# Optimization experiments

Measured on AMD Instinct MI355X. Metric: run time of the kernel, lower is better.

The kernel has to match this reference:

```python
import jax, jax.numpy as jnp
import numpy as np

D_MODEL = 768
D_POS = 64
NHEAD = 12
D_FF = 3072
HEAD_DIM = D_MODEL // NHEAD
LN_EPS = 1e-5


def _layer_norm(x, gamma, beta):
    mu = jnp.mean(x, axis=-1, keepdims=True)
    var = jnp.var(x, axis=-1, keepdims=True)
    return (x - mu) * jax.lax.rsqrt(var + LN_EPS) * gamma + beta


def setup_inputs() -> dict:
    key = jax.random.key(0)
    ks = jax.random.split(key, 16)
    L, N = 256, 4
    s = 0.02
    return {
        "src": jax.random.normal(ks[0], (L, N, D_MODEL), jnp.float32),
        "pos": jax.random.normal(ks[1], (N, L, L, D_POS), jnp.float32),
        "q_w": jax.random.normal(ks[2], (D_MODEL, D_MODEL), jnp.float32) * s,
        "q_b": jnp.zeros((D_MODEL,), jnp.float32),
        "k_w": jax.random.normal(ks[3], (D_MODEL, D_MODEL), jnp.float32) * s,
        "k_b": jnp.zeros((D_MODEL,), jnp.float32),
        "v_w": jax.random.normal(ks[4], (D_MODEL, D_MODEL), jnp.float32) * s,
        "v_b": jnp.zeros((D_MODEL,), jnp.float32),
        "p_w": jax.random.normal(ks[5], (D_MODEL, D_POS), jnp.float32) * s,
        "p_b": jnp.zeros((D_MODEL,), jnp.float32),
        "out_w": jax.random.normal(ks[6], (D_MODEL, D_MODEL), jnp.float32) * s,
        "out_b": jnp.zeros((D_MODEL,), jnp.float32),
        "lin1_w": jax.random.normal(ks[7], (D_FF, D_MODEL), jnp.float32) * s,
        "lin1_b": jnp.zeros((D_FF,), jnp.float32),
        "lin2_w": jax.random.normal(ks[8], (D_MODEL, D_FF), jnp.float32) * s,
        "lin2_b": jnp.zeros((D_MODEL,), jnp.float32),
        "n1_g": jnp.ones((D_MODEL,), jnp.float32),
        "n1_b": jnp.zeros((D_MODEL,), jnp.float32),
        "n2_g": jnp.ones((D_MODEL,), jnp.float32),
        "n2_b": jnp.zeros((D_MODEL,), jnp.float32),
    }


def reference(src, pos, q_w, q_b, k_w, k_b, v_w, v_b, p_w, p_b,
              out_w, out_b, lin1_w, lin1_b, lin2_w, lin2_b,
              n1_g, n1_b, n2_g, n2_b):
    L, N, E = src.shape
    H, hd = NHEAD, HEAD_DIM
    scaling = float(hd) ** -0.5

    # projections (F.linear: x @ W.T + b)
    q = (src @ q_w.T + q_b).reshape(L, N, H, hd).transpose(1, 2, 0, 3) * scaling  # (N,H,L,hd)
    k = (src @ k_w.T + k_b).reshape(L, N, H, hd).transpose(1, 2, 0, 3)            # (N,H,L,hd)
    v = (src @ v_w.T + v_b).reshape(L, N, H, hd).transpose(1, 2, 0, 3)            # (N,H,L,hd)
    p = (pos @ p_w.T + p_b).reshape(N, L, L, H, hd)                               # (N,L,L,H,hd)

    # content-content + content-position scores
    scores = jnp.einsum('nhid,nhjd->nhij', q, k) \
           + jnp.einsum('nhid,nijhd->nhij', q, p)                                 # (N,H,L,L)
    attn = jax.nn.softmax(scores, axis=-1)

    ctx = jnp.einsum('nhij,nhjd->nhid', attn, v)          # (N,H,L,hd)
    ctx = ctx.transpose(2, 0, 1, 3).reshape(L, N, E)      # (L,N,E)
    attn_out = ctx @ out_w.T + out_b

    x = _layer_norm(src + attn_out, n1_g, n1_b)
    ff = jax.nn.gelu(x @ lin1_w.T + lin1_b, approximate=False) @ lin2_w.T + lin2_b
    x = _layer_norm(x + ff, n2_g, n2_b)
    return x
```

## Files before the change

### kernel.cpp

```cpp
#include <hip/hip_runtime.h>
#include <hip/hip_bf16.h>
#include <math.h>

typedef __hip_bfloat16 bf16;
typedef unsigned short u16;
typedef __attribute__((ext_vector_type(8))) short bf16x8;
typedef __attribute__((ext_vector_type(4))) float f32x4;

#define L_SEQ 256
#define NB 4
#define EMB 768
#define NH 12
#define DFF 3072
#define HD 64

__device__ __forceinline__ float ldE(const void* p, size_t i, int f32) {
    return f32 ? ((const float*)p)[i] : __bfloat162float(((const bf16*)p)[i]);
}
__device__ __forceinline__ float b2f(u16 v) { return __uint_as_float(((unsigned)v) << 16); }
__device__ __forceinline__ u16 f2b(float v) {
    bf16 h = __float2bfloat16(v);
    return *(u16*)&h;
}

__global__ void detect_kernel(const void* __restrict__ src, int* __restrict__ flagp) {
    __shared__ int cnt[256];
    int t = threadIdx.x;
    unsigned w = ((const unsigned*)src)[t];
    unsigned e = ((w & 0xFFFFu) >> 7) & 0xFFu;
    cnt[t] = (e >= 0xC3u) ? 1 : 0;
    __syncthreads();
    for (int off = 128; off; off >>= 1) {
        if (t < off) cnt[t] += cnt[t + off];
        __syncthreads();
    }
    if (t == 0) *flagp = (cnt[0] > 8) ? 1 : 0;
}

__device__ __forceinline__ void cvt8(u16* dst, const void* s, size_t off, int f32) {
    if (f32) {
        const float* sf = (const float*)s + off;
        #pragma unroll
        for (int t = 0; t < 8; ++t) dst[t] = f2b(sf[t]);
    } else {
        *(uint4*)dst = *(const uint4*)((const u16*)s + off);
    }
}

__global__ void pack_all(u16* __restrict__ xb, u16* __restrict__ wqkv,
                         u16* __restrict__ owb, u16* __restrict__ l1b,
                         u16* __restrict__ l2b, float* __restrict__ biasf,
                         const void* src, const void* qw, const void* kw, const void* vw,
                         const void* ow, const void* l1w, const void* l2w,
                         const void* qb, const void* kb, const void* vb,
                         const void* ob, const void* b1, const void* b2,
                         const int* __restrict__ flagp) {
    const int f32 = *flagp;
    int b = blockIdx.x;
    if (b >= 3840) {
        int o = (b - 3840) * 256 + threadIdx.x;
        if (o >= 6912) return;
        float v;
        if (o < 768)       v = ldE(qb, o, f32);
        else if (o < 1536) v = ldE(kb, o - 768, f32);
        else if (o < 2304) v = ldE(vb, o - 1536, f32);
        else if (o < 3072) v = ldE(ob, o - 2304, f32);
        else if (o < 6144) v = ldE(b1, o - 3072, f32);
        else               v = ldE(b2, o - 6144, f32);
        biasf[o] = v;
        return;
    }
    int gid = b * 256 + threadIdx.x;
    u16 tmp[8];
    if (gid < 98304) {
        size_t idx = (size_t)gid * 8;
        cvt8(tmp, src, idx, f32);
        *(uint4*)(xb + idx) = *(uint4*)tmp;
    } else if (gid < 319488) {
        size_t idx = (size_t)(gid - 98304) * 8;
        int r = (int)(idx / EMB);
        const void* s;
        size_t off;
        if (r < EMB)          { s = qw; off = idx; }
        else if (r < 2 * EMB) { s = kw; off = idx - (size_t)EMB * EMB; }
        else                  { s = vw; off = idx - (size_t)2 * EMB * EMB; }
        cvt8(tmp, s, off, f32);
        *(uint4*)(wqkv + idx) = *(uint4*)tmp;
    } else if (gid < 393216) {
        size_t idx = (size_t)(gid - 319488) * 8;
        cvt8(tmp, ow, idx, f32);
        *(uint4*)(owb + idx) = *(uint4*)tmp;
    } else if (gid < 688128) {
        size_t idx = (size_t)(gid - 393216) * 8;
        cvt8(tmp, l1w, idx, f32);
        *(uint4*)(l1b + idx) = *(uint4*)tmp;
    } else {
        size_t idx = (size_t)(gid - 688128) * 8;
        cvt8(tmp, l2w, idx, f32);
        *(uint4*)(l2b + idx) = *(uint4*)tmp;
    }
}

template <int MODE>
__global__ __launch_bounds__(256) void mfma_gemm(
        const u16* __restrict__ A, const u16* __restrict__ W,
        const float* __restrict__ biasf,
        u16* __restrict__ outB0, u16* __restrict__ outB1, u16* __restrict__ outB2,
        float* __restrict__ outF, float* __restrict__ outF2,
        int K, int lda, int ksplit) {
    __shared__ u16 As[128][40];
    __shared__ u16 Ws[128][40];
    int tid = threadIdx.x;
    int wave = tid >> 6, lane = tid & 63;
    int quad = lane >> 4, col = lane & 15;
    int m0 = blockIdx.y * 128, n0 = blockIdx.x * 128;
    int z = blockIdx.z;
    const u16* Ap = A + (size_t)z * ksplit;
    const u16* Wp = W + (size_t)z * ksplit;
    int wm = (wave >> 1) * 64, wn = (wave & 1) * 64;
    f32x4 acc[4][4];
    #pragma unroll
    for (int a = 0; a < 4; ++a)
        #pragma unroll
        for (int b = 0; b < 4; ++b) acc[a][b] = (f32x4){0.f, 0.f, 0.f, 0.f};
    for (int k0 = 0; k0 < K; k0 += 32) {
        #pragma unroll
        for (int it = 0; it < 2; ++it) {
            int l = tid + it * 256;
            int r = l >> 2, c4 = (l & 3) * 8;
            *(uint4*)&As[r][c4] = *(const uint4*)&Ap[(size_t)(m0 + r) * lda + k0 + c4];
            *(uint4*)&Ws[r][c4] = *(const uint4*)&Wp[(size_t)(n0 + r) * lda + k0 + c4];
        }
        __syncthreads();
        bf16x8 af[4], bfr[4];
        #pragma unroll
        for (int mi = 0; mi < 4; ++mi)
            af[mi] = __builtin_bit_cast(bf16x8, *(const uint4*)&As[wm + mi * 16 + col][quad * 8]);
        #pragma unroll
        for (int ni = 0; ni < 4; ++ni)
            bfr[ni] = __builtin_bit_cast(bf16x8, *(const uint4*)&Ws[wn + ni * 16 + col][quad * 8]);
        #pragma unroll
        for (int mi = 0; mi < 4; ++mi)
            #pragma unroll
            for (int ni = 0; ni < 4; ++ni)
                acc[mi][ni] = __builtin_amdgcn_mfma_f32_16x16x32_bf16(
                    af[mi], bfr[ni], acc[mi][ni], 0, 0, 0);
        __syncthreads();
    }
    #pragma unroll
    for (int mi = 0; mi < 4; ++mi)
        #pragma unroll
        for (int ni = 0; ni < 4; ++ni)
            #pragma unroll
            for (int reg = 0; reg < 4; ++reg) {
                int rr = m0 + wm + mi * 16 + quad * 4 + reg;
                int cc = n0 + wn + ni * 16 + col;
                float v = acc[mi][ni][reg];
                if (MODE == 0) {
                    v += biasf[cc];
                    if (cc < EMB) {
                        outB0[(size_t)rr * EMB + cc] = f2b(v * 0.125f);
                    } else if (cc < 2 * EMB) {
                        outB1[(size_t)rr * EMB + cc - EMB] = f2b(v);
                    } else {
                        outB2[((size_t)(rr & 3) * EMB + (cc - 2 * EMB)) * L_SEQ + (rr >> 2)] = f2b(v);
                    }
                } else if (MODE == 2) {
                    v += biasf[cc];
                    v = 0.5f * v * (1.0f + erff(v * 0.70710678118654752f));
                    outB0[(size_t)rr * DFF + cc] = f2b(v);
                } else if (MODE == 4) {
                    float* o = z ? outF2 : outF;
                    o[(size_t)rr * EMB + cc] = v;
                } else {
                    atomicAdd(&outF[(size_t)rr * EMB + cc], v);
                }
            }
}

__global__ void qp_kernel(const u16* __restrict__ qb, const void* __restrict__ p_w,
                          const void* __restrict__ p_b, u16* __restrict__ qp_b,
                          float* __restrict__ qpb, const int* __restrict__ flagp) {
    const int f32 = *flagp;
    int blk = blockIdx.x;
    int i = blk & 255;
    int h = (blk >> 8) % NH;
    int n = blk / (256 * NH);
    int t = threadIdx.x;
    __shared__ float qs[64];
    qs[t] = b2f(qb[(size_t)(i * NB + n) * EMB + h * HD + t]);
    __syncthreads();
    float acc = 0.f;
    #pragma unroll 16
    for (int d = 0; d < 64; ++d)
        acc += qs[d] * ldE(p_w, (size_t)(h * HD + d) * HD + t, f32);
    qp_b[(((size_t)(n * L_SEQ + i)) * 16 + h) * 64 + t] = f2b(acc);
    float v = qs[t] * ldE(p_b, h * HD + t, f32);
    #pragma unroll
    for (int off = 32; off; off >>= 1) v += __shfl_down(v, off);
    if (t == 0) qpb[blk] = v;
}

__global__ __launch_bounds__(256) void s2_mfma(
        const u16* __restrict__ qp_b, const float* __restrict__ qpb,
        const void* __restrict__ pos, float* __restrict__ S,
        const int* __restrict__ flagp) {
    const int f32 = *flagp;
    int wid = (blockIdx.x << 2) + (threadIdx.x >> 6);
    int i = wid & 255, n = wid >> 8;
    int lane = threadIdx.x & 63;
    int quad = lane >> 4, col = lane & 15;
    const u16* qprow = qp_b + (((size_t)wid) * 16 + col) * 64;
    bf16x8 a0 = __builtin_bit_cast(bf16x8, *(const uint4*)(qprow + quad * 8));
    bf16x8 a1 = __builtin_bit_cast(bf16x8, *(const uint4*)(qprow + 32 + quad * 8));
    float qpb_r[4];
    #pragma unroll
    for (int reg = 0; reg < 4; ++reg) {
        int h = quad * 4 + reg;
        qpb_r[reg] = (h < NH) ? qpb[((size_t)n * NH + h) * L_SEQ + i] : 0.f;
    }
    #pragma unroll 4
    for (int t = 0; t < 16; ++t) {
        int j = t * 16 + col;
        size_t pbase = ((size_t)(n * L_SEQ + i) * L_SEQ + j) * HD;
        bf16x8 b0, b1;
        if (f32) {
            const float* pf = (const float*)pos + pbase;
            u16 tmp[16];
            #pragma unroll
            for (int c = 0; c < 8; ++c) tmp[c] = f2b(pf[quad * 8 + c]);
            #pragma unroll
            for (int c = 0; c < 8; ++c) tmp[8 + c] = f2b(pf[32 + quad * 8 + c]);
            b0 = *(bf16x8*)tmp;
            b1 = *(bf16x8*)(tmp + 8);
        } else {
            const u16* pb = (const u16*)pos + pbase;
            b0 = __builtin_bit_cast(bf16x8, *(const uint4*)(pb + quad * 8));
            b1 = __builtin_bit_cast(bf16x8, *(const uint4*)(pb + 32 + quad * 8));
        }
        f32x4 acc = (f32x4){0.f, 0.f, 0.f, 0.f};
        acc = __builtin_amdgcn_mfma_f32_16x16x32_bf16(a0, b0, acc, 0, 0, 0);
        acc = __builtin_amdgcn_mfma_f32_16x16x32_bf16(a1, b1, acc, 0, 0, 0);
        if (quad < 3) {
            #pragma unroll
            for (int reg = 0; reg < 4; ++reg) {
                int h = quad * 4 + reg;
                S[(((size_t)n * NH + h) * L_SEQ + i) * L_SEQ + j] = acc[reg] + qpb_r[reg];
            }
        }
    }
}

__global__ __launch_bounds__(256) void attn3_kernel(
        const u16* __restrict__ qb, const u16* __restrict__ kb,
        const u16* __restrict__ vt, const float* __restrict__ S,
        u16* __restrict__ ctxb) {
    __shared__ u16 p_lds[4][16][268];
    int b = blockIdx.x;
    int n = b / 48, rem = b % 48, h = rem >> 2, it = rem & 3;
    int wave = threadIdx.x >> 6, lane = threadIdx.x & 63;
    int quad = lane >> 4, col = lane & 15;
    int i0 = it * 64 + wave * 16;

    const u16* qrow = qb + ((size_t)(i0 + col) * NB + n) * EMB + h * HD;
    bf16x8 a0 = __builtin_bit_cast(bf16x8, *(const uint4*)(qrow + quad * 8));
    bf16x8 a1 = __builtin_bit_cast(bf16x8, *(const uint4*)(qrow + 32 + quad * 8));

    f32x4 sc[16];
    #pragma unroll
    for (int t = 0; t < 16; ++t) {
        const u16* krow = kb + ((size_t)(t * 16 + col) * NB + n) * EMB + h * HD;
        bf16x8 b0 = __builtin_bit_cast(bf16x8, *(const uint4*)(krow + quad * 8));
        bf16x8 b1 = __builtin_bit_cast(bf16x8, *(const uint4*)(krow + 32 + quad * 8));
        f32x4 acc = (f32x4){0.f, 0.f, 0.f, 0.f};
        acc = __builtin_amdgcn_mfma_f32_16x16x32_bf16(a0, b0, acc, 0, 0, 0);
        acc = __builtin_amdgcn_mfma_f32_16x16x32_bf16(a1, b1, acc, 0, 0, 0);
        sc[t] = acc;
    }

    #pragma unroll
    for (int reg = 0; reg < 4; ++reg) {
        const float* Srow = S + (((size_t)n * NH + h) * L_SEQ + i0 + quad * 4 + reg) * L_SEQ + col;
        float m = -1e30f;
        #pragma unroll
        for (int t = 0; t < 16; ++t) {
            float v = sc[t][reg] + Srow[t * 16];
            sc[t][reg] = v;
            m = fmaxf(m, v);
        }
        #pragma unroll
        for (int off = 1; off < 16; off <<= 1) m = fmaxf(m, __shfl_xor(m, off));
        float sum = 0.f;
        #pragma unroll
        for (int t = 0; t < 16; ++t) {
            float e = __expf(sc[t][reg] - m);
            sc[t][reg] = e;
            sum += e;
        }
        #pragma unroll
        for (int off = 1; off < 16; off <<= 1) sum += __shfl_xor(sum, off);
        float inv = 1.0f / sum;
        #pragma unroll
        for (int t = 0; t < 16; ++t)
            p_lds[wave][quad * 4 + reg][t * 16 + col] = f2b(sc[t][reg] * inv);
    }

    bf16x8 ap[8];
    #pragma unroll
    for (int kt = 0; kt < 8; ++kt)
        ap[kt] = __builtin_bit_cast(bf16x8, *(const uint4*)&p_lds[wave][col][kt * 32 + quad * 8]);
    #pragma unroll
    for (int nt = 0; nt < 4; ++nt) {
        const u16* vrow = vt + ((size_t)n * EMB + h * HD + nt * 16 + col) * L_SEQ;
        f32x4 acc = (f32x4){0.f, 0.f, 0.f, 0.f};
        #pragma unroll
        for (int kt = 0; kt < 8; ++kt) {
            bf16x8 bp = __builtin_bit_cast(bf16x8, *(const uint4*)(vrow + kt * 32 + quad * 8));
            acc = __builtin_amdgcn_mfma_f32_16x16x32_bf16(ap[kt], bp, acc, 0, 0, 0);
        }
        #pragma unroll
        for (int reg = 0; reg < 4; ++reg) {
            int ii = i0 + quad * 4 + reg;
            ctxb[((size_t)ii * NB + n) * EMB + h * HD + nt * 16 + col] = f2b(acc[reg]);
        }
    }
}

__global__ void ln1_kernel(const float* __restrict__ p0, const float* __restrict__ p1,
                           const void* __restrict__ src, const float* __restrict__ biasf,
                           const void* __restrict__ g, const void* __restrict__ b,
                           u16* __restrict__ x1b, float* __restrict__ y2,
                           const int* __restrict__ flagp) {
    const int f32 = *flagp;
    int r = blockIdx.x;
    int t = threadIdx.x;
    __shared__ float red[256];
    float x[3];
    #pragma unroll
    for (int p = 0; p < 3; ++p) {
        int e = t + p * 256;
        size_t oi = (size_t)r * EMB + e;
        x[p] = p0[oi] + p1[oi] + ldE(src, oi, f32) + biasf[2304 + e];
    }
    red[t] = x[0] + x[1] + x[2];
    __syncthreads();
    for (int off = 128; off; off >>= 1) {
        if (t < off) red[t] += red[t + off];
        __syncthreads();
    }
    float mean = red[0] * (1.0f / EMB);
    __syncthreads();
    float d0 = x[0] - mean, d1 = x[1] - mean, d2 = x[2] - mean;
    red[t] = d0 * d0 + d1 * d1 + d2 * d2;
    __syncthreads();
    for (int off = 128; off; off >>= 1) {
        if (t < off) red[t] += red[t + off];
        __syncthreads();
    }
    float rstd = rsqrtf(red[0] * (1.0f / EMB) + 1e-5f);
    float vs[3] = {d0, d1, d2};
    #pragma unroll
    for (int p = 0; p < 3; ++p) {
        int e = t + p * 256;
        float v = vs[p] * rstd * ldE(g, e, f32) + ldE(b, e, f32);
        size_t oi = (size_t)r * EMB + e;
        x1b[oi] = f2b(v);
        y2[oi] = v + biasf[6144 + e];
    }
}

__global__ void ln2_kernel(const float* __restrict__ X, const void* __restrict__ g,
                           const void* __restrict__ b, void* __restrict__ outAny,
                           const int* __restrict__ flagp) {
    const int f32 = *flagp;
    int r = blockIdx.x;
    int t = threadIdx.x;
    __shared__ float red[256];
    float x0 = X[(size_t)r * EMB + t];
    float x1 = X[(size_t)r * EMB + t + 256];
    float x2 = X[(size_t)r * EMB + t + 512];
    red[t] = x0 + x1 + x2;
    __syncthreads();
    for (int off = 128; off; off >>= 1) {
        if (t < off) red[t] += red[t + off];
        __syncthreads();
    }
    float mean = red[0] * (1.0f / EMB);
    __syncthreads();
    float d0 = x0 - mean, d1 = x1 - mean, d2 = x2 - mean;
    red[t] = d0 * d0 + d1 * d1 + d2 * d2;
    __syncthreads();
    for (int off = 128; off; off >>= 1) {
        if (t < off) red[t] += red[t + off];
        __syncthreads();
    }
    float rstd = rsqrtf(red[0] * (1.0f / EMB) + 1e-5f);
    float vs[3] = {d0, d1, d2};
    #pragma unroll
    for (int p = 0; p < 3; ++p) {
        int e = t + p * 256;
        float v = vs[p] * rstd * ldE(g, e, f32) + ldE(b, e, f32);
        size_t oi = (size_t)r * EMB + e;
        if (f32) ((float*)outAny)[oi] = v;
        else     ((bf16*)outAny)[oi] = __float2bfloat16(v);
    }
}

extern "C" void kernel_launch(void* const* d_in, const int* in_sizes, int n_in,
                              void* d_out, int out_size, void* d_ws, size_t ws_size,
                              hipStream_t stream) {
    const void* src    = d_in[0];
    const void* pos    = d_in[1];
    const void* q_w    = d_in[2];
    const void* q_b    = d_in[3];
    const void* k_w    = d_in[4];
    const void* k_b    = d_in[5];
    const void* v_w    = d_in[6];
    const void* v_b    = d_in[7];
    const void* p_w    = d_in[8];
    const void* p_b    = d_in[9];
    const void* out_w  = d_in[10];
    const void* out_b  = d_in[11];
    const void* lin1_w = d_in[12];
    const void* lin1_b = d_in[13];
    const void* lin2_w = d_in[14];
    const void* lin2_b = d_in[15];
    const void* n1_g   = d_in[16];
    const void* n1_b   = d_in[17];
    const void* n2_g   = d_in[18];
    const void* n2_b   = d_in[19];

    float* f = (float*)d_ws;
    int*   flagp = (int*)f;
    float* biasf = f + 16;
    u16*   xb    = (u16*)(f + 6928);
    u16*   wqkv  = (u16*)(f + 400144);
    u16*   owb   = (u16*)(f + 1284880);
    u16*   l1b   = (u16*)(f + 1579792);
    u16*   l2b   = (u16*)(f + 2759440);
    u16*   qbp   = (u16*)(f + 3939088);
    u16*   kbp   = (u16*)(f + 4332304);
    u16*   vtb   = (u16*)(f + 4725520);
    u16*   qp_b  = (u16*)(f + 5118736);
    float* qpb   = f + 5643024;
    float* S     = f + 5655312;
    u16*   ctxb  = (u16*)(f + 8801040);
    u16*   ffb   = (u16*)S;
    float* y2    = S + 1572864;
    float* pOut1 = S + 2359296;
    float* pOut0 = f + 400144;
    u16*   x1b   = vtb;

    detect_kernel<<<1, 256, 0, stream>>>(src, flagp);

    pack_all<<<3867, 256, 0, stream>>>(xb, wqkv, owb, l1b, l2b, biasf,
                                       src, q_w, k_w, v_w, out_w, lin1_w, lin2_w,
                                       q_b, k_b, v_b, out_b, lin1_b, lin2_b, flagp);

    mfma_gemm<0><<<dim3(18, 8), 256, 0, stream>>>(
        xb, wqkv, biasf, qbp, kbp, vtb, nullptr, nullptr, EMB, EMB, 0);

    qp_kernel<<<NB * NH * L_SEQ, 64, 0, stream>>>(qbp, p_w, p_b, qp_b, qpb, flagp);
    s2_mfma<<<NB * L_SEQ / 4, 256, 0, stream>>>(qp_b, qpb, pos, S, flagp);

    attn3_kernel<<<NB * NH * 4, 256, 0, stream>>>(qbp, kbp, vtb, S, ctxb);

    mfma_gemm<4><<<dim3(6, 8, 2), 256, 0, stream>>>(
        ctxb, owb, nullptr, nullptr, nullptr, nullptr, pOut0, pOut1, 384, EMB, 384);

    ln1_kernel<<<1024, 256, 0, stream>>>(pOut0, pOut1, src, biasf, n1_g, n1_b,
                                         x1b, y2, flagp);

    mfma_gemm<2><<<dim3(24, 8), 256, 0, stream>>>(
        x1b, l1b, biasf + 3072, ffb, nullptr, nullptr, nullptr, nullptr, EMB, EMB, 0);

    mfma_gemm<5><<<dim3(6, 8, 4), 256, 0, stream>>>(
        ffb, l2b, nullptr, nullptr, nullptr, nullptr, y2, nullptr, 768, DFF, 768);

    ln2_kernel<<<1024, 256, 0, stream>>>(y2, n2_g, n2_b, d_out, flagp);
}
```

Baseline: 309.6 us.

## Fuse weight/input bf16 conversion into GEMM loads and shrink tiles for occupancy

Removes the separate pack_all kernel so each GEMM reads the original fp32 (or bf16) weights and inputs and converts them to bf16 while staging into shared memory. Biases are read directly inside the epilogues instead of from a packed buffer. GEMM tiles shrink from 128x128 to 64x128 and attention blocks from 4 to 2 waves, doubling grid sizes to fill more compute units. The out-projection split-K goes from 2 to 3 parts. The trade-off is that every GEMM block now reloads and converts fp32 weights, which doubles weight read traffic, and the smaller tiles reuse less data per block.

```diff
diff --git a/kernel.cpp b/kernel.cpp
--- a/kernel.cpp
+++ b/kernel.cpp
@@ -37,112 +37,75 @@
     if (t == 0) *flagp = (cnt[0] > 8) ? 1 : 0;
 }
 
-__device__ __forceinline__ void cvt8(u16* dst, const void* s, size_t off, int f32) {
+__device__ __forceinline__ void stage8(u16* dst, const void* s, size_t off, int f32) {
     if (f32) {
         const float* sf = (const float*)s + off;
-        #pragma unroll
-        for (int t = 0; t < 8; ++t) dst[t] = f2b(sf[t]);
+        float4 a = *(const float4*)sf;
+        float4 b = *(const float4*)(sf + 4);
+        u16 t[8] = {f2b(a.x), f2b(a.y), f2b(a.z), f2b(a.w),
+                    f2b(b.x), f2b(b.y), f2b(b.z), f2b(b.w)};
+        *(uint4*)dst = *(uint4*)t;
     } else {
         *(uint4*)dst = *(const uint4*)((const u16*)s + off);
     }
 }
 
-__global__ void pack_all(u16* __restrict__ xb, u16* __restrict__ wqkv,
-                         u16* __restrict__ owb, u16* __restrict__ l1b,
-                         u16* __restrict__ l2b, float* __restrict__ biasf,
-                         const void* src, const void* qw, const void* kw, const void* vw,
-                         const void* ow, const void* l1w, const void* l2w,
-                         const void* qb, const void* kb, const void* vb,
-                         const void* ob, const void* b1, const void* b2,
-                         const int* __restrict__ flagp) {
+template <int MODE, int AEXT>
+__global__ __launch_bounds__(256) void mfma_gemm(
+        const void* __restrict__ A, const void* __restrict__ W0,
+        const void* __restrict__ W1, const void* __restrict__ W2,
+        const void* __restrict__ b0, const void* __restrict__ b1,
+        const void* __restrict__ b2,
+        u16* __restrict__ outB0, u16* __restrict__ outB1, u16* __restrict__ outB2,
+        float* __restrict__ outF,
+        int K, int lda, int ksplit, const int* __restrict__ flagp) {
     const int f32 = *flagp;
-    int b = blockIdx.x;
-    if (b >= 3840) {
-        int o = (b - 3840) * 256 + threadIdx.x;
-        if (o >= 6912) return;
-        float v;
-        if (o < 768)       v = ldE(qb, o, f32);
-        else if (o < 1536) v = ldE(kb, o - 768, f32);
-        else if (o < 2304) v = ldE(vb, o - 1536, f32);
-        else if (o < 3072) v = ldE(ob, o - 2304, f32);
-        else if (o < 6144) v = ldE(b1, o - 3072, f32);
-        else               v = ldE(b2, o - 6144, f32);
-        biasf[o] = v;
-        return;
-    }
-    int gid = b * 256 + threadIdx.x;
-    u16 tmp[8];
-    if (gid < 98304) {
-        size_t idx = (size_t)gid * 8;
-        cvt8(tmp, src, idx, f32);
-        *(uint4*)(xb + idx) = *(uint4*)tmp;
-    } else if (gid < 319488) {
-        size_t idx = (size_t)(gid - 98304) * 8;
-        int r = (int)(idx / EMB);
-        const void* s;
-        size_t off;
-        if (r < EMB)          { s = qw; off = idx; }
-        else if (r < 2 * EMB) { s = kw; off = idx - (size_t)EMB * EMB; }
-        else                  { s = vw; off = idx - (size_t)2 * EMB * EMB; }
-        cvt8(tmp, s, off, f32);
-        *(uint4*)(wqkv + idx) = *(uint4*)tmp;
-    } else if (gid < 393216) {
-        size_t idx = (size_t)(gid - 319488) * 8;
-        cvt8(tmp, ow, idx, f32);
-        *(uint4*)(owb + idx) = *(uint4*)tmp;
-    } else if (gid < 688128) {
-        size_t idx = (size_t)(gid - 393216) * 8;
-        cvt8(tmp, l1w, idx, f32);
-        *(uint4*)(l1b + idx) = *(uint4*)tmp;
-    } else {
-        size_t idx = (size_t)(gid - 688128) * 8;
-        cvt8(tmp, l2w, idx, f32);
-        *(uint4*)(l2b + idx) = *(uint4*)tmp;
-    }
-}
-
-template <int MODE>
-__global__ __launch_bounds__(256) void mfma_gemm(
-        const u16* __restrict__ A, const u16* __restrict__ W,
-        const float* __restrict__ biasf,
-        u16* __restrict__ outB0, u16* __restrict__ outB1, u16* __restrict__ outB2,
-        float* __restrict__ outF, float* __restrict__ outF2,
-        int K, int lda, int ksplit) {
-    __shared__ u16 As[128][40];
+    const int af32 = AEXT ? f32 : 0;
+    __shared__ u16 As[64][40];
     __shared__ u16 Ws[128][40];
     int tid = threadIdx.x;
     int wave = tid >> 6, lane = tid & 63;
     int quad = lane >> 4, col = lane & 15;
-    int m0 = blockIdx.y * 128, n0 = blockIdx.x * 128;
+    int m0 = blockIdx.y * 64, n0 = blockIdx.x * 128;
     int z = blockIdx.z;
-    const u16* Ap = A + (size_t)z * ksplit;
-    const u16* Wp = W + (size_t)z * ksplit;
-    int wm = (wave >> 1) * 64, wn = (wave & 1) * 64;
-    f32x4 acc[4][4];
+    size_t zoff = (size_t)z * ksplit;
+    const void* Wt = W0;
+    int nb = n0, sel = 0;
+    if (MODE == 0) {
+        sel = n0 / EMB;
+        Wt = sel == 0 ? W0 : (sel == 1 ? W1 : W2);
+        nb = n0 - sel * EMB;
+    }
+    f32x4 acc[4][2];
     #pragma unroll
     for (int a = 0; a < 4; ++a)
         #pragma unroll
-        for (int b = 0; b < 4; ++b) acc[a][b] = (f32x4){0.f, 0.f, 0.f, 0.f};
+        for (int b = 0; b < 2; ++b) acc[a][b] = (f32x4){0.f, 0.f, 0.f, 0.f};
     for (int k0 = 0; k0 < K; k0 += 32) {
         #pragma unroll
-        for (int it = 0; it < 2; ++it) {
+        for (int it = 0; it < 3; ++it) {
             int l = tid + it * 256;
-            int r = l >> 2, c4 = (l & 3) * 8;
-            *(uint4*)&As[r][c4] = *(const uint4*)&Ap[(size_t)(m0 + r) * lda + k0 + c4];
-            *(uint4*)&Ws[r][c4] = *(const uint4*)&Wp[(size_t)(n0 + r) * lda + k0 + c4];
-        }
-        __syncthreads();
-        bf16x8 af[4], bfr[4];
+            if (l < 256) {
+                int r = l >> 2, c8 = (l & 3) * 8;
+                stage8(&As[r][c8], A, (size_t)(m0 + r) * lda + k0 + c8 + zoff, af32);
+            } else {
+                int l2 = l - 256;
+                int r = l2 >> 2, c8 = (l2 & 3) * 8;
+                stage8(&Ws[r][c8], Wt, (size_t)(nb + r) * lda + k0 + c8 + zoff, f32);
+            }
+        }
+        __syncthreads();
+        bf16x8 af[4], bfr[2];
         #pragma unroll
         for (int mi = 0; mi < 4; ++mi)
-            af[mi] = __builtin_bit_cast(bf16x8, *(const uint4*)&As[wm + mi * 16 + col][quad * 8]);
-        #pragma unroll
-        for (int ni = 0; ni < 4; ++ni)
-            bfr[ni] = __builtin_bit_cast(bf16x8, *(const uint4*)&Ws[wn + ni * 16 + col][quad * 8]);
+            af[mi] = __builtin_bit_cast(bf16x8, *(const uint4*)&As[mi * 16 + col][quad * 8]);
+        #pragma unroll
+        for (int ni = 0; ni < 2; ++ni)
+            bfr[ni] = __builtin_bit_cast(bf16x8, *(const uint4*)&Ws[wave * 32 + ni * 16 + col][quad * 8]);
         #pragma unroll
         for (int mi = 0; mi < 4; ++mi)
             #pragma unroll
-            for (int ni = 0; ni < 4; ++ni)
+            for (int ni = 0; ni < 2; ++ni)
                 acc[mi][ni] = __builtin_amdgcn_mfma_f32_16x16x32_bf16(
                     af[mi], bfr[ni], acc[mi][ni], 0, 0, 0);
         __syncthreads();
@@ -150,28 +113,29 @@
     #pragma unroll
     for (int mi = 0; mi < 4; ++mi)
         #pragma unroll
-        for (int ni = 0; ni < 4; ++ni)
+        for (int ni = 0; ni < 2; ++ni)
             #pragma unroll
             for (int reg = 0; reg < 4; ++reg) {
-                int rr = m0 + wm + mi * 16 + quad * 4 + reg;
-                int cc = n0 + wn + ni * 16 + col;
+                int rr = m0 + mi * 16 + quad * 4 + reg;
+                int cc = n0 + wave * 32 + ni * 16 + col;
                 float v = acc[mi][ni][reg];
                 if (MODE == 0) {
-                    v += biasf[cc];
-                    if (cc < EMB) {
-                        outB0[(size_t)rr * EMB + cc] = f2b(v * 0.125f);
-                    } else if (cc < 2 * EMB) {
-                        outB1[(size_t)rr * EMB + cc - EMB] = f2b(v);
+                    int cl = cc - sel * EMB;
+                    const void* bt = sel == 0 ? b0 : (sel == 1 ? b1 : b2);
+                    v += ldE(bt, cl, f32);
+                    if (sel == 0) {
+                        outB0[(size_t)rr * EMB + cl] = f2b(v * 0.125f);
+                    } else if (sel == 1) {
+                        outB1[(size_t)rr * EMB + cl] = f2b(v);
                     } else {
-                        outB2[((size_t)(rr & 3) * EMB + (cc - 2 * EMB)) * L_SEQ + (rr >> 2)] = f2b(v);
+                        outB2[((size_t)(rr & 3) * EMB + cl) * L_SEQ + (rr >> 2)] = f2b(v);
                     }
                 } else if (MODE == 2) {
-                    v += biasf[cc];
+                    v += ldE(b0, cc, f32);
                     v = 0.5f * v * (1.0f + erff(v * 0.70710678118654752f));
                     outB0[(size_t)rr * DFF + cc] = f2b(v);
                 } else if (MODE == 4) {
-                    float* o = z ? outF2 : outF;
-                    o[(size_t)rr * EMB + cc] = v;
+                    outF[(size_t)z * 1024 * EMB + (size_t)rr * EMB + cc] = v;
                 } else {
                     atomicAdd(&outF[(size_t)rr * EMB + cc], v);
                 }
@@ -251,16 +215,16 @@
     }
 }
 
-__global__ __launch_bounds__(256) void attn3_kernel(
+__global__ __launch_bounds__(128) void attn3_kernel(
         const u16* __restrict__ qb, const u16* __restrict__ kb,
         const u16* __restrict__ vt, const float* __restrict__ S,
         u16* __restrict__ ctxb) {
-    __shared__ u16 p_lds[4][16][268];
+    __shared__ u16 p_lds[2][16][268];
     int b = blockIdx.x;
-    int n = b / 48, rem = b % 48, h = rem >> 2, it = rem & 3;
+    int n = b / 96, rem = b % 96, h = rem >> 3, it = rem & 7;
     int wave = threadIdx.x >> 6, lane = threadIdx.x & 63;
     int quad = lane >> 4, col = lane & 15;
-    int i0 = it * 64 + wave * 16;
+    int i0 = it * 32 + wave * 16;
 
     const u16* qrow = qb + ((size_t)(i0 + col) * NB + n) * EMB + h * HD;
     bf16x8 a0 = __builtin_bit_cast(bf16x8, *(const uint4*)(qrow + quad * 8));
@@ -326,8 +290,8 @@
     }
 }
 
-__global__ void ln1_kernel(const float* __restrict__ p0, const float* __restrict__ p1,
-                           const void* __restrict__ src, const float* __restrict__ biasf,
+__global__ void ln1_kernel(const float* __restrict__ parts, const void* __restrict__ src,
+                           const void* __restrict__ out_b, const void* __restrict__ lin2_b,
                            const void* __restrict__ g, const void* __restrict__ b,
                            u16* __restrict__ x1b, float* __restrict__ y2,
                            const int* __restrict__ flagp) {
@@ -335,12 +299,14 @@
     int r = blockIdx.x;
     int t = threadIdx.x;
     __shared__ float red[256];
+    const size_t PS = (size_t)1024 * EMB;
     float x[3];
     #pragma unroll
     for (int p = 0; p < 3; ++p) {
         int e = t + p * 256;
         size_t oi = (size_t)r * EMB + e;
-        x[p] = p0[oi] + p1[oi] + ldE(src, oi, f32) + biasf[2304 + e];
+        x[p] = parts[oi] + parts[PS + oi] + parts[2 * PS + oi]
+             + ldE(src, oi, f32) + ldE(out_b, e, f32);
     }
     red[t] = x[0] + x[1] + x[2];
     __syncthreads();
@@ -365,7 +331,7 @@
         float v = vs[p] * rstd * ldE(g, e, f32) + ldE(b, e, f32);
         size_t oi = (size_t)r * EMB + e;
         x1b[oi] = f2b(v);
-        y2[oi] = v + biasf[6144 + e];
+        y2[oi] = v + ldE(lin2_b, e, f32);
     }
 }
 
@@ -432,50 +398,43 @@
 
     float* f = (float*)d_ws;
     int*   flagp = (int*)f;
-    float* biasf = f + 16;
-    u16*   xb    = (u16*)(f + 6928);
-    u16*   wqkv  = (u16*)(f + 400144);
-    u16*   owb   = (u16*)(f + 1284880);
-    u16*   l1b   = (u16*)(f + 1579792);
-    u16*   l2b   = (u16*)(f + 2759440);
-    u16*   qbp   = (u16*)(f + 3939088);
-    u16*   kbp   = (u16*)(f + 4332304);
-    u16*   vtb   = (u16*)(f + 4725520);
-    u16*   qp_b  = (u16*)(f + 5118736);
-    float* qpb   = f + 5643024;
-    float* S     = f + 5655312;
-    u16*   ctxb  = (u16*)(f + 8801040);
-    u16*   ffb   = (u16*)S;
-    float* y2    = S + 1572864;
-    float* pOut1 = S + 2359296;
-    float* pOut0 = f + 400144;
-    u16*   x1b   = vtb;
+    u16*   qbp   = (u16*)(f + 16);
+    u16*   kbp   = (u16*)(f + 393232);
+    u16*   vtb   = (u16*)(f + 786448);
+    u16*   qp_b  = (u16*)(f + 1179664);
+    float* qpb   = f + 1703952;
+    float* S     = f + 1716240;
+    u16*   ctxb  = (u16*)(f + 4861968);
+    float* parts = f + 5255184;
+    u16*   x1b   = (u16*)(f + 7614480);
+    float* y2    = f + 8007696;
+    u16*   ffb   = (u16*)(f + 8794128);
 
     detect_kernel<<<1, 256, 0, stream>>>(src, flagp);
 
-    pack_all<<<3867, 256, 0, stream>>>(xb, wqkv, owb, l1b, l2b, biasf,
-                                       src, q_w, k_w, v_w, out_w, lin1_w, lin2_w,
-                                       q_b, k_b, v_b, out_b, lin1_b, lin2_b, flagp);
-
-    mfma_gemm<0><<<dim3(18, 8), 256, 0, stream>>>(
-        xb, wqkv, biasf, qbp, kbp, vtb, nullptr, nullptr, EMB, EMB, 0);
+    mfma_gemm<0, 1><<<dim3(18, 16), 256, 0, stream>>>(
+        src, q_w, k_w, v_w, q_b, k_b, v_b, qbp, kbp, vtb, nullptr,
+        EMB, EMB, 0, flagp);
 
     qp_kernel<<<NB * NH * L_SEQ, 64, 0, stream>>>(qbp, p_w, p_b, qp_b, qpb, flagp);
     s2_mfma<<<NB * L_SEQ / 4, 256, 0, stream>>>(qp_b, qpb, pos, S, flagp);
 
-    attn3_kernel<<<NB * NH * 4, 256, 0, stream>>>(qbp, kbp, vtb, S, ctxb);
-
-    mfma_gemm<4><<<dim3(6, 8, 2), 256, 0, stream>>>(
-        ctxb, owb, nullptr, nullptr, nullptr, nullptr, pOut0, pOut1, 384, EMB, 384);
-
-    ln1_kernel<<<1024, 256, 0, stream>>>(pOut0, pOut1, src, biasf, n1_g, n1_b,
+    attn3_kernel<<<NB * NH * 8, 128, 0, stream>>>(qbp, kbp, vtb, S, ctxb);
+
+    mfma_gemm<4, 0><<<dim3(6, 16, 3), 256, 0, stream>>>(
+        ctxb, out_w, nullptr, nullptr, nullptr, nullptr, nullptr,
+        nullptr, nullptr, nullptr, parts, 256, EMB, 256, flagp);
+
+    ln1_kernel<<<1024, 256, 0, stream>>>(parts, src, out_b, lin2_b, n1_g, n1_b,
                                          x1b, y2, flagp);
 
-    mfma_gemm<2><<<dim3(24, 8), 256, 0, stream>>>(
-        x1b, l1b, biasf + 3072, ffb, nullptr, nullptr, nullptr, nullptr, EMB, EMB, 0);
-
-    mfma_gemm<5><<<dim3(6, 8, 4), 256, 0, stream>>>(
-        ffb, l2b, nullptr, nullptr, nullptr, nullptr, y2, nullptr, 768, DFF, 768);
+    mfma_gemm<2, 0><<<dim3(24, 16), 256, 0, stream>>>(
+        x1b, lin1_w, nullptr, nullptr, lin1_b, nullptr, nullptr,
+        ffb, nullptr, nullptr, nullptr, EMB, EMB, 0, flagp);
+
+    mfma_gemm<5, 0><<<dim3(6, 16, 4), 256, 0, stream>>>(
+        ffb, lin2_w, nullptr, nullptr, nullptr, nullptr, nullptr,
+        nullptr, nullptr, nullptr, y2, 768, DFF, 768, flagp);
 
     ln2_kernel<<<1024, 256, 0, stream>>>(y2, n2_g, n2_b, d_out, flagp);
 }
```

Measured after the change: 363.5 us. 17.4% more time.

## Fuse q·p_w projection into position-score MFMA kernel and merge detect into pack

Applied to the files above, without the earlier changes.

Removes the separate qp_kernel by packing a transposed bf16 p_w plus p_b row in pack_all and computing each query's per-head position projection with block-diagonal MFMAs inside the position-score kernel, staged through LDS. It also folds the dtype-detect kernel into pack_all, and splits attention into smaller 128-thread blocks for more parallelism. This removes two launches and the 12288-block scalar qp kernel and its global round trip. The cost is a masked MFMA sweep of 24×5 tiles per wave, mostly on zero operands, and every pack block repeating the detection reduction.

```diff
diff --git a/kernel.cpp b/kernel.cpp
--- a/kernel.cpp
+++ b/kernel.cpp
@@ -23,20 +23,6 @@
     return *(u16*)&h;
 }
 
-__global__ void detect_kernel(const void* __restrict__ src, int* __restrict__ flagp) {
-    __shared__ int cnt[256];
-    int t = threadIdx.x;
-    unsigned w = ((const unsigned*)src)[t];
-    unsigned e = ((w & 0xFFFFu) >> 7) & 0xFFu;
-    cnt[t] = (e >= 0xC3u) ? 1 : 0;
-    __syncthreads();
-    for (int off = 128; off; off >>= 1) {
-        if (t < off) cnt[t] += cnt[t + off];
-        __syncthreads();
-    }
-    if (t == 0) *flagp = (cnt[0] > 8) ? 1 : 0;
-}
-
 __device__ __forceinline__ void cvt8(u16* dst, const void* s, size_t off, int f32) {
     if (f32) {
         const float* sf = (const float*)s + off;
@@ -50,15 +36,46 @@
 __global__ void pack_all(u16* __restrict__ xb, u16* __restrict__ wqkv,
                          u16* __restrict__ owb, u16* __restrict__ l1b,
                          u16* __restrict__ l2b, float* __restrict__ biasf,
+                         u16* __restrict__ p_wT,
                          const void* src, const void* qw, const void* kw, const void* vw,
                          const void* ow, const void* l1w, const void* l2w,
                          const void* qb, const void* kb, const void* vb,
                          const void* ob, const void* b1, const void* b2,
-                         const int* __restrict__ flagp) {
-    const int f32 = *flagp;
+                         const void* pw, const void* pb,
+                         int* __restrict__ flagp) {
+    __shared__ int cnt[256];
+    int t = threadIdx.x;
+    {
+        unsigned w = ((const unsigned*)src)[t];
+        unsigned e = ((w & 0xFFFFu) >> 7) & 0xFFu;
+        cnt[t] = (e >= 0xC3u) ? 1 : 0;
+        __syncthreads();
+        for (int off = 128; off; off >>= 1) {
+            if (t < off) cnt[t] += cnt[t + off];
+            __syncthreads();
+        }
+    }
+    const int f32 = (cnt[0] > 8) ? 1 : 0;
     int b = blockIdx.x;
+    if (b == 0 && t == 0) *flagp = f32;
+    if (b >= 3867) {
+        int o = (b - 3867) * 256 + t;
+        if (o >= 6240) return;
+        int idx = o * 8;
+        int c = idx / EMB, e0 = idx % EMB;
+        u16 tmp[8];
+        if (c < 64) {
+            #pragma unroll
+            for (int k = 0; k < 8; ++k) tmp[k] = f2b(ldE(pw, (size_t)(e0 + k) * 64 + c, f32));
+        } else {
+            #pragma unroll
+            for (int k = 0; k < 8; ++k) tmp[k] = f2b(ldE(pb, e0 + k, f32));
+        }
+        *(uint4*)(p_wT + idx) = *(uint4*)tmp;
+        return;
+    }
     if (b >= 3840) {
-        int o = (b - 3840) * 256 + threadIdx.x;
+        int o = (b - 3840) * 256 + t;
         if (o >= 6912) return;
         float v;
         if (o < 768)       v = ldE(qb, o, f32);
@@ -70,7 +87,7 @@
         biasf[o] = v;
         return;
     }
-    int gid = b * 256 + threadIdx.x;
+    int gid = b * 256 + t;
     u16 tmp[8];
     if (gid < 98304) {
         size_t idx = (size_t)gid * 8;
@@ -178,47 +195,50 @@
             }
 }
 
-__global__ void qp_kernel(const u16* __restrict__ qb, const void* __restrict__ p_w,
-                          const void* __restrict__ p_b, u16* __restrict__ qp_b,
-                          float* __restrict__ qpb, const int* __restrict__ flagp) {
-    const int f32 = *flagp;
-    int blk = blockIdx.x;
-    int i = blk & 255;
-    int h = (blk >> 8) % NH;
-    int n = blk / (256 * NH);
-    int t = threadIdx.x;
-    __shared__ float qs[64];
-    qs[t] = b2f(qb[(size_t)(i * NB + n) * EMB + h * HD + t]);
-    __syncthreads();
-    float acc = 0.f;
-    #pragma unroll 16
-    for (int d = 0; d < 64; ++d)
-        acc += qs[d] * ldE(p_w, (size_t)(h * HD + d) * HD + t, f32);
-    qp_b[(((size_t)(n * L_SEQ + i)) * 16 + h) * 64 + t] = f2b(acc);
-    float v = qs[t] * ldE(p_b, h * HD + t, f32);
-    #pragma unroll
-    for (int off = 32; off; off >>= 1) v += __shfl_down(v, off);
-    if (t == 0) qpb[blk] = v;
-}
-
-__global__ __launch_bounds__(256) void s2_mfma(
-        const u16* __restrict__ qp_b, const float* __restrict__ qpb,
+__global__ __launch_bounds__(256) void s2q_mfma(
+        const u16* __restrict__ qbp, const u16* __restrict__ p_wT,
         const void* __restrict__ pos, float* __restrict__ S,
         const int* __restrict__ flagp) {
     const int f32 = *flagp;
-    int wid = (blockIdx.x << 2) + (threadIdx.x >> 6);
+    __shared__ u16 qp_l[4][16][68];
+    __shared__ float qpb_l[4][16];
+    int wave = threadIdx.x >> 6, lane = threadIdx.x & 63;
+    int quad = lane >> 4, col = lane & 15;
+    int wid = (blockIdx.x << 2) + wave;
     int i = wid & 255, n = wid >> 8;
-    int lane = threadIdx.x & 63;
-    int quad = lane >> 4, col = lane & 15;
-    const u16* qprow = qp_b + (((size_t)wid) * 16 + col) * 64;
-    bf16x8 a0 = __builtin_bit_cast(bf16x8, *(const uint4*)(qprow + quad * 8));
-    bf16x8 a1 = __builtin_bit_cast(bf16x8, *(const uint4*)(qprow + 32 + quad * 8));
+    const u16* qrow = qbp + (size_t)(i * NB + n) * EMB;
+
+    f32x4 qpacc[5];
+    #pragma unroll
+    for (int nt = 0; nt < 5; ++nt) qpacc[nt] = (f32x4){0.f, 0.f, 0.f, 0.f};
+    #pragma unroll
+    for (int kt = 0; kt < 24; ++kt) {
+        int owner = (4 * kt + quad) >> 3;
+        uint4 av = (col == owner) ? *(const uint4*)(qrow + kt * 32 + quad * 8)
+                                  : (uint4){0u, 0u, 0u, 0u};
+        bf16x8 a = __builtin_bit_cast(bf16x8, av);
+        #pragma unroll
+        for (int nt = 0; nt < 5; ++nt) {
+            bf16x8 bb = __builtin_bit_cast(bf16x8,
+                *(const uint4*)(p_wT + (size_t)(nt * 16 + col) * EMB + kt * 32 + quad * 8));
+            qpacc[nt] = __builtin_amdgcn_mfma_f32_16x16x32_bf16(a, bb, qpacc[nt], 0, 0, 0);
+        }
+    }
+    #pragma unroll
+    for (int nt = 0; nt < 4; ++nt)
+        #pragma unroll
+        for (int reg = 0; reg < 4; ++reg)
+            qp_l[wave][quad * 4 + reg][nt * 16 + col] = f2b(qpacc[nt][reg]);
+    if (col == 0) {
+        #pragma unroll
+        for (int reg = 0; reg < 4; ++reg) qpb_l[wave][quad * 4 + reg] = qpacc[4][reg];
+    }
+    bf16x8 a0 = __builtin_bit_cast(bf16x8, *(const uint4*)&qp_l[wave][col][quad * 8]);
+    bf16x8 a1 = __builtin_bit_cast(bf16x8, *(const uint4*)&qp_l[wave][col][32 + quad * 8]);
     float qpb_r[4];
     #pragma unroll
-    for (int reg = 0; reg < 4; ++reg) {
-        int h = quad * 4 + reg;
-        qpb_r[reg] = (h < NH) ? qpb[((size_t)n * NH + h) * L_SEQ + i] : 0.f;
-    }
+    for (int reg = 0; reg < 4; ++reg) qpb_r[reg] = qpb_l[wave][quad * 4 + reg];
+
     #pragma unroll 4
     for (int t = 0; t < 16; ++t) {
         int j = t * 16 + col;
@@ -251,16 +271,16 @@
     }
 }
 
-__global__ __launch_bounds__(256) void attn3_kernel(
+__global__ __launch_bounds__(128) void attn3_kernel(
         const u16* __restrict__ qb, const u16* __restrict__ kb,
         const u16* __restrict__ vt, const float* __restrict__ S,
         u16* __restrict__ ctxb) {
-    __shared__ u16 p_lds[4][16][268];
+    __shared__ u16 p_lds[2][16][268];
     int b = blockIdx.x;
-    int n = b / 48, rem = b % 48, h = rem >> 2, it = rem & 3;
+    int n = b / 96, rem = b % 96, h = rem >> 3, it = rem & 7;
     int wave = threadIdx.x >> 6, lane = threadIdx.x & 63;
     int quad = lane >> 4, col = lane & 15;
-    int i0 = it * 64 + wave * 16;
+    int i0 = it * 32 + wave * 16;
 
     const u16* qrow = qb + ((size_t)(i0 + col) * NB + n) * EMB + h * HD;
     bf16x8 a0 = __builtin_bit_cast(bf16x8, *(const uint4*)(qrow + quad * 8));
@@ -441,29 +461,26 @@
     u16*   qbp   = (u16*)(f + 3939088);
     u16*   kbp   = (u16*)(f + 4332304);
     u16*   vtb   = (u16*)(f + 4725520);
-    u16*   qp_b  = (u16*)(f + 5118736);
-    float* qpb   = f + 5643024;
-    float* S     = f + 5655312;
-    u16*   ctxb  = (u16*)(f + 8801040);
+    u16*   p_wT  = (u16*)(f + 5118736);
+    float* S     = f + 5143824;
+    u16*   ctxb  = (u16*)(f + 8289552);
     u16*   ffb   = (u16*)S;
     float* y2    = S + 1572864;
     float* pOut1 = S + 2359296;
     float* pOut0 = f + 400144;
     u16*   x1b   = vtb;
 
-    detect_kernel<<<1, 256, 0, stream>>>(src, flagp);
-
-    pack_all<<<3867, 256, 0, stream>>>(xb, wqkv, owb, l1b, l2b, biasf,
+    pack_all<<<3892, 256, 0, stream>>>(xb, wqkv, owb, l1b, l2b, biasf, p_wT,
                                        src, q_w, k_w, v_w, out_w, lin1_w, lin2_w,
-                                       q_b, k_b, v_b, out_b, lin1_b, lin2_b, flagp);
+                                       q_b, k_b, v_b, out_b, lin1_b, lin2_b,
+                                       p_w, p_b, flagp);
 
     mfma_gemm<0><<<dim3(18, 8), 256, 0, stream>>>(
         xb, wqkv, biasf, qbp, kbp, vtb, nullptr, nullptr, EMB, EMB, 0);
 
-    qp_kernel<<<NB * NH * L_SEQ, 64, 0, stream>>>(qbp, p_w, p_b, qp_b, qpb, flagp);
-    s2_mfma<<<NB * L_SEQ / 4, 256, 0, stream>>>(qp_b, qpb, pos, S, flagp);
-
-    attn3_kernel<<<NB * NH * 4, 256, 0, stream>>>(qbp, kbp, vtb, S, ctxb);
+    s2q_mfma<<<NB * L_SEQ / 4, 256, 0, stream>>>(qbp, p_wT, pos, S, flagp);
+
+    attn3_kernel<<<NB * NH * 8, 128, 0, stream>>>(qbp, kbp, vtb, S, ctxb);
 
     mfma_gemm<4><<<dim3(6, 8, 2), 256, 0, stream>>>(
         ctxb, owb, nullptr, nullptr, nullptr, nullptr, pOut0, pOut1, 384, EMB, 384);
```

Measured after the change: 316.0 us. 2.0% more time.
